# Kernel optimization log

Hardware: AMD Instinct MI355X
Metric: run time of the kernel (lower is better)

Reference implementation:

```python
import jax, jax.numpy as jnp
import numpy as np

B, T = 16, 512
S = T - 16  # sequence length after three 5x5 VALID convs and pool (H: T-4-4-4-5+1)
H = 64      # GRU hidden size


def setup_inputs() -> dict:
    key = jax.random.key(0)
    ks = jax.random.split(key, 20)
    def prm(k, shape, s=0.02):
        return jax.random.normal(k, shape, dtype=jnp.float32) * s
    return {
        "evaluation": jax.random.normal(ks[0], (B, 128, T), dtype=jnp.float32),
        "template":   jax.random.normal(ks[1], (B, 128, T), dtype=jnp.float32),
        "conv1_w": prm(ks[2], (16, 1, 5, 5), 0.05),  "conv1_b": prm(ks[3], (16,)),
        "conv2_w": prm(ks[4], (32, 16, 5, 5), 0.05), "conv2_b": prm(ks[5], (32,)),
        "conv3_w": prm(ks[6], (64, 32, 5, 5), 0.05), "conv3_b": prm(ks[7], (64,)),
        "lin1_w": prm(ks[8], (64, 3712)), "lin1_b": prm(ks[9], (64,)),
        "W_ih": prm(ks[10], (192, 64), 0.1), "W_hh": prm(ks[11], (192, 64), 0.1),
        "b_ih": prm(ks[12], (192,)),          "b_hh": prm(ks[13], (192,)),
        "att_w": prm(ks[14], (1, 64)),  "att_b": prm(ks[15], (1,)),
        "lin3_w": prm(ks[16], (128, 64)), "lin3_b": prm(ks[17], (128,)),
        "cls_w": prm(ks[18], (2, 128)),   "cls_b": prm(ks[19], (2,)),
    }


def _conv(x, w, b):
    # x: (N, C, H, W), w: (O, C, kh, kw), VALID, stride 1
    y = jax.lax.conv_general_dilated(x, w, (1, 1), 'VALID',
                                     dimension_numbers=('NCHW', 'OIHW', 'NCHW'))
    return y + b[None, :, None, None]


def _gru_seq(x, W_ih, W_hh, b_ih, b_hh):
    # x: (L, 64). One hidden state carried over the whole length (this mirrors
    # the torch module threading h0/h1 across samples in its Python loop).
    gi = x @ W_ih.T + b_ih  # (L, 192) input gates precomputed
    def step(h, gi_t):
        gh = W_hh @ h + b_hh
        r = jax.nn.sigmoid(gi_t[:H] + gh[:H])
        z = jax.nn.sigmoid(gi_t[H:2 * H] + gh[H:2 * H])
        n = jnp.tanh(gi_t[2 * H:] + r * gh[2 * H:])
        h_new = (1.0 - z) * n + z * h
        return h_new, h_new
    _, hs = jax.lax.scan(step, jnp.zeros((H,), x.dtype), gi)
    return hs  # (L, 64)


def reference(evaluation, template, conv1_w, conv1_b, conv2_w, conv2_b,
              conv3_w, conv3_b, lin1_w, lin1_b, W_ih, W_hh, b_ih, b_hh,
              att_w, att_b, lin3_w, lin3_b, cls_w, cls_b):
    # Shared conv trunk on stacked eval+template batch
    x = jnp.concatenate([evaluation, template], axis=0)      # (2B, 128, T)
    x = jnp.transpose(x, (0, 2, 1))[:, None]                 # (2B, 1, T, 128)
    x = _conv(x, conv1_w, conv1_b)                           # (2B, 16, T-4, 124)
    x = _conv(x, conv2_w, conv2_b)                           # (2B, 32, T-8, 120)
    x = _conv(x, conv3_w, conv3_b)                           # (2B, 64, T-12, 116)
    x = jax.lax.reduce_window(x, -jnp.inf, jax.lax.max,
                              (1, 1, 5, 2), (1, 1, 1, 2), 'VALID')  # (2B, 64, S, 58)
    # torch does a raw per-sample reshape (64, S, 58) -> (S, 3712)
    x = x.reshape(2 * B, S, 3712)
    x = x @ lin1_w.T + lin1_b                                # (2B, S, 64)
    # GRU: hidden carried across the batch -> one long scan per branch
    E = _gru_seq(x[:B].reshape(B * S, H), W_ih, W_hh, b_ih, b_hh).reshape(B, S, H)
    Tm = _gru_seq(x[B:].reshape(B * S, H), W_ih, W_hh, b_ih, b_hh).reshape(B, S, H)
    # alignment_weights[m, n] = <E[m], Tm[n]>, softmax over m (dim=0 per sample)
    A = jax.nn.softmax(jnp.einsum('bmd,bnd->bmn', E, Tm), axis=1)
    Tp = jnp.einsum('bmn,bnd->bmd', A, Tm)                   # template_prim
    dist = jnp.abs(Tp - E)                                    # (B, S, 64)
    att = jax.nn.softmax(jnp.einsum('bsd,d->bs', E, att_w[0]) + att_b[0], axis=1)
    rep = jnp.einsum('bs,bsd->bd', att, dist)                 # (B, 64)
    h = jax.nn.relu(rep)
    h = jax.nn.relu(h @ lin3_w.T + lin3_b)
    return h @ cls_w.T + cls_b                                # (B, 2)
```

## Files before the change

kernel.cpp:

```cpp
#include <hip/hip_runtime.h>
#include <hip/hip_bf16.h>
#include <math.h>


#define DEVI static __device__ __forceinline__
typedef __attribute__((ext_vector_type(8))) short short8;
typedef __attribute__((ext_vector_type(4))) float f32x4;
typedef __attribute__((ext_vector_type(8))) float f32x8;
typedef unsigned short ushort_t;

DEVI float fsig(float x)   { return 1.f / (1.f + __expf(-x)); }
DEVI float ftanh_(float x) { return 2.f / (1.f + __expf(-2.f * x)) - 1.f; }
DEVI float bf2f(ushort_t u) { union { unsigned int i; float f; } v; v.i = ((unsigned int)u) << 16; return v.f; }
DEVI ushort_t f2bf(float f) {
    union { float f; unsigned int i; } v; v.f = f;
    unsigned int r = v.i + 0x7FFF + ((v.i >> 16) & 1);
    return (ushort_t)(r >> 16);
}
DEVI f32x8 bf2f8(short8 s) {
    f32x8 r;
#pragma unroll
    for (int k = 0; k < 8; k++) r[k] = bf2f((ushort_t)s[k]);
    return r;
}
DEVI f32x8 max8(f32x8 a, f32x8 b) {
    f32x8 r;
#pragma unroll
    for (int k = 0; k < 8; k++) r[k] = fmaxf(a[k], b[k]);
    return r;
}

DEVI void glds16(const ushort_t* g, ushort_t* l)
{
    __builtin_amdgcn_global_load_lds(
        (const __attribute__((address_space(1))) void*)g,
        (__attribute__((address_space(3))) void*)l, 16, 0, 0);
}

__global__ void pack_w2(const float* __restrict__ w2, ushort_t* __restrict__ w2p)
{
    for (int idx = blockIdx.x * 256 + threadIdx.x; idx < 15360; idx += gridDim.x * 256) {
        int kh = idx / 3072, rem = idx % 3072;
        int kw = rem / 512;
        int co = (rem >> 4) & 31, ci = rem & 15;
        float v = (kw < 5) ? w2[((co * 16 + ci) * 5 + kh) * 5 + kw] : 0.f;
        w2p[idx] = f2bf(v);
    }
}
__global__ void pack_w3(const float* __restrict__ w3, ushort_t* __restrict__ w3p)
{
    for (int idx = blockIdx.x * 256 + threadIdx.x; idx < 51200; idx += gridDim.x * 256) {
        int kh = idx / 10240, rem = idx % 10240;
        int kw = rem / 2048;
        int co = (rem >> 5) & 63, ci = rem & 31;
        w3p[idx] = f2bf(w3[((co * 32 + ci) * 5 + kh) * 5 + kw]);
    }
}
__global__ void pack_l1w(const float* __restrict__ l1w, ushort_t* __restrict__ l1wp)
{
    for (int idx = blockIdx.x * 256 + threadIdx.x; idx < 262144; idx += gridDim.x * 256) {
        int n = idx >> 12, kp = idx & 4095;
        int r = kp >> 6, j = kp & 63;
        float v = (j < 58) ? l1w[n * 3712 + r * 58 + j] : 0.f;
        l1wp[idx] = f2bf(v);
    }
}

__global__ void conv1_kernel(const float* __restrict__ ev,
                             const float* __restrict__ tmpl,
                             const float* __restrict__ wgt,
                             const float* __restrict__ bias,
                             ushort_t* __restrict__ out, int n0)
{
    const int h0  = blockIdx.x * 4;
    const int w0  = blockIdx.y * 62;
    const int nl  = blockIdx.z;
    const int n   = n0 + nl;
    const int tid = threadIdx.x;
    const int wl  = tid & 63;
    const int cg  = tid >> 6;
    const float* src = (n < 16) ? (ev + (size_t)n * 65536)
                                : (tmpl + (size_t)(n - 16) * 65536);

    __shared__ float tin[8 * 68];
    __shared__ float tw[16 * 25];

    float acc[4][4];
#pragma unroll
    for (int j = 0; j < 4; j++)
#pragma unroll
        for (int hh = 0; hh < 4; hh++) acc[j][hh] = 0.f;

    for (int idx = tid; idx < 528; idx += 256) {
        int cc = idx >> 3, r = idx & 7;
        tin[r * 68 + cc] = src[(w0 + cc) * 512 + h0 + r];
    }
    for (int idx = tid; idx < 400; idx += 256) tw[idx] = wgt[idx];
    __syncthreads();
#pragma unroll
    for (int kh = 0; kh < 5; kh++) {
#pragma unroll
        for (int kw = 0; kw < 5; kw++) {
            float iv[4];
#pragma unroll
            for (int hh = 0; hh < 4; hh++)
                iv[hh] = tin[(hh + kh) * 68 + wl + kw];
#pragma unroll
            for (int j = 0; j < 4; j++) {
                float wv = tw[(cg * 4 + j) * 25 + kh * 5 + kw];
#pragma unroll
                for (int hh = 0; hh < 4; hh++)
                    acc[j][hh] = fmaf(wv, iv[hh], acc[j][hh]);
            }
        }
    }
    if (wl < 62) {
#pragma unroll
        for (int hh = 0; hh < 4; hh++) {
            ushort_t pk[4];
#pragma unroll
            for (int j = 0; j < 4; j++)
                pk[j] = f2bf(acc[j][hh] + bias[cg * 4 + j]);
            ushort_t* dst = out + ((size_t)(nl * 508 + h0 + hh) * 124 + w0 + wl) * 16 + cg * 4;
            *(uint2*)dst = *(uint2*)pk;
        }
    }
}

template<int CI, int CO, int NF, int MF, int NHI, int W_T, int KSTEPS,
         int KW_TOT, int H_IN, int W_IN, bool PAD2, bool HPOOL, int MAXB>
__global__ __launch_bounds__(256, MAXB) void conv_mfma(
    const ushort_t* __restrict__ in, const ushort_t* __restrict__ wpk,
    const float* __restrict__ bias, ushort_t* __restrict__ out)
{
    constexpr int H_OUT = H_IN - 4;
    constexpr int W_OUT = W_IN - 4;
    constexpr int HALO  = W_T + 6;
    constexpr int OCT   = CI / 8;
    constexpr int AROWS = 4 * NHI + 4;
    constexpr int APL   = AROWS * HALO;
    constexpr int BPL   = KW_TOT * CO;

    const int h0 = blockIdx.x * (4 * NHI);
    const int w0 = blockIdx.y * W_T;
    const int nl = blockIdx.z;
    const int tid  = threadIdx.x;
    const int wv   = tid >> 6;
    const int lane = tid & 63;
    const int l16  = lane & 15;
    const int kq   = lane >> 4;

    __shared__ __align__(16) ushort_t As[OCT * APL * 8];
    __shared__ __align__(16) ushort_t Bs[OCT * BPL * 8];

    f32x4 acc[NHI][MF][NF];
#pragma unroll
    for (int hi = 0; hi < NHI; hi++)
#pragma unroll
        for (int mi = 0; mi < MF; mi++)
#pragma unroll
            for (int ni = 0; ni < NF; ni++)
                acc[hi][mi][ni] = f32x4{0.f, 0.f, 0.f, 0.f};

    for (int idx = tid; idx < OCT * APL; idx += 256) {
        int oct = idx / APL, e = idx - oct * APL;
        int r = e / HALO, c = e - r * HALO;
        glds16(in + ((size_t)((nl * H_IN + h0 + r) * W_IN + w0 + c)) * CI + oct * 8,
               &As[idx * 8]);
    }

    const int aoct = PAD2 ? (kq & 1) : kq;
    const int kwq  = PAD2 ? (kq >> 1) : 0;

#pragma unroll
    for (int kh = 0; kh < 5; kh++) {
        __syncthreads();
        for (int idx = tid; idx < OCT * BPL; idx += 256) {
            int oct = idx / BPL, e = idx - oct * BPL;
            int kw = e / CO, co = e - kw * CO;
            glds16(wpk + ((size_t)((kh * KW_TOT + kw) * CO + co)) * CI + oct * 8,
                   &Bs[idx * 8]);
        }
        __syncthreads();
#pragma unroll
        for (int st = 0; st < KSTEPS; st++) {
            const int colq = (PAD2 ? st * 2 : st) + kwq;
            short8 bfv[NF];
#pragma unroll
            for (int ni = 0; ni < NF; ni++)
                bfv[ni] = *(const short8*)&Bs[(aoct * BPL + colq * CO + ni * 16 + l16) * 8];
#pragma unroll
            for (int hi = 0; hi < NHI; hi++) {
                short8 af[MF];
#pragma unroll
                for (int mi = 0; mi < MF; mi++)
                    af[mi] = *(const short8*)&As[(aoct * APL + (hi * 4 + wv + kh) * HALO + mi * 16 + l16 + colq) * 8];
#pragma unroll
                for (int mi = 0; mi < MF; mi++)
#pragma unroll
                    for (int ni = 0; ni < NF; ni++)
                        acc[hi][mi][ni] = __builtin_amdgcn_mfma_f32_16x16x32_bf16(
                            af[mi], bfv[ni], acc[hi][mi][ni], 0, 0, 0);
            }
        }
    }

#pragma unroll
    for (int hi = 0; hi < NHI; hi++) {
        const int h = h0 + hi * 4 + wv;
        if (h < H_OUT) {
#pragma unroll
            for (int mi = 0; mi < MF; mi++) {
#pragma unroll
                for (int ni = 0; ni < NF; ni++) {
                    int co = ni * 16 + l16;
                    float bv = bias[co];
                    if constexpr (HPOOL) {
                        const int jw = (w0 + mi * 16 + kq * 4) >> 1;
                        if (jw < 58)
                            out[((size_t)(nl * H_OUT + h) * 58 + jw) * CO + co] =
                                f2bf(fmaxf(acc[hi][mi][ni][0], acc[hi][mi][ni][1]) + bv);
                        if (jw + 1 < 58)
                            out[((size_t)(nl * H_OUT + h) * 58 + jw + 1) * CO + co] =
                                f2bf(fmaxf(acc[hi][mi][ni][2], acc[hi][mi][ni][3]) + bv);
                    } else {
#pragma unroll
                        for (int reg = 0; reg < 4; reg++) {
                            int w = w0 + mi * 16 + kq * 4 + reg;
                            if (w < W_OUT)
                                out[((size_t)(nl * H_OUT + h) * W_OUT + w) * CO + co] =
                                    f2bf(acc[hi][mi][ni][reg] + bv);
                        }
                    }
                }
            }
        }
    }
}

__global__ __launch_bounds__(512) void pool_fused(const ushort_t* __restrict__ a3h,
                                                  ushort_t* __restrict__ pooled)
{
    const int nl = blockIdx.y;
    const int s0 = blockIdx.x * 16;
    const int t  = threadIdx.x;
    __shared__ ushort_t L[4 * 3712];

    const int j = t >> 3, oct = t & 7;
    const ushort_t* base = a3h + (size_t)nl * 1856000 + (size_t)j * 64 + oct * 8;
    ushort_t* dst = pooled + (size_t)nl * 1841152;

#define LOADROW(rr) bf2f8(*(const short8*)(base + (size_t)(rr) * 3712))
    f32x8 w0, w1, w2v, w3v;
    if (t < 464) {
        w0  = LOADROW(s0);
        w1  = LOADROW(s0 + 1);
        w2v = LOADROW(s0 + 2);
        w3v = LOADROW(s0 + 3);
    }
    for (int g = 0; g < 4; g++) {
        if (t < 464) {
#pragma unroll
            for (int k = 0; k < 4; k++) {
                int s = s0 + g * 4 + k;
                f32x8 w4 = LOADROW(s + 4);
                f32x8 mx = max8(max8(max8(w0, w1), max8(w2v, w3v)), w4);
#pragma unroll
                for (int u = 0; u < 8; u++)
                    L[k * 3712 + (oct * 8 + u) * 58 + j] = f2bf(mx[u]);
                w0 = w1; w1 = w2v; w2v = w3v; w3v = w4;
            }
        }
        __syncthreads();
        const int sg = s0 + g * 4;
        for (int e = t; e < 14848; e += 512) {
            int k = e / 3712, r = e - k * 3712;
            int c = r / 58, jj = r - c * 58;
            dst[(size_t)c * 28768 + (sg + k) * 58 + jj] = L[e];
        }
        __syncthreads();
    }
#undef LOADROW
}

__global__ __launch_bounds__(256) void lin1_mfma(
    const ushort_t* __restrict__ pooled, const ushort_t* __restrict__ l1wp,
    float* __restrict__ xb, int n0, int RT)
{
    const int mt  = blockIdx.x;
    const int kqb = blockIdx.y;
    const int r0  = mt * 64;
    const int t   = threadIdx.x;
    const int wv  = t >> 6, lane = t & 63, l16 = lane & 15, kq = lane >> 4;

    __shared__ __align__(16) ushort_t As[8 * 64 * 8];
    __shared__ __align__(16) ushort_t Bs[8 * 64 * 8];

    f32x4 acc[4];
#pragma unroll
    for (int ni = 0; ni < 4; ni++) acc[ni] = f32x4{0.f, 0.f, 0.f, 0.f};

    for (int kb = 0; kb < 16; kb++) {
        const int k0 = kqb * 1024 + kb * 64;
        const int r  = k0 >> 6;
        __syncthreads();
        for (int idx = t; idx < 512; idx += 256) {
            int oct = idx >> 6, row = idx & 63;
            int rr = r0 + row;
            short8 v = short8{0, 0, 0, 0, 0, 0, 0, 0};
            if (rr < RT)
                v = *(const short8*)(pooled + (size_t)rr * 3712 + r * 58 + oct * 8);
            *(short8*)&As[idx * 8] = v;
        }
        for (int idx = t; idx < 512; idx += 256) {
            int oct = idx >> 6, co = idx & 63;
            *(short8*)&Bs[idx * 8] =
                *(const short8*)(l1wp + (size_t)co * 4096 + k0 + oct * 8);
        }
        __syncthreads();
#pragma unroll
        for (int st = 0; st < 2; st++) {
            short8 af = *(const short8*)&As[((st * 4 + kq) * 64 + wv * 16 + l16) * 8];
#pragma unroll
            for (int ni = 0; ni < 4; ni++) {
                short8 bfv = *(const short8*)&Bs[((st * 4 + kq) * 64 + ni * 16 + l16) * 8];
                acc[ni] = __builtin_amdgcn_mfma_f32_16x16x32_bf16(af, bfv, acc[ni], 0, 0, 0);
            }
        }
    }
#pragma unroll
    for (int ni = 0; ni < 4; ni++) {
        int co = ni * 16 + l16;
#pragma unroll
        for (int reg = 0; reg < 4; reg++) {
            int rr = r0 + wv * 16 + kq * 4 + reg;
            if (rr < RT)
                atomicAdd(&xb[((size_t)n0 * 496 + rr) * 64 + co], acc[ni][reg]);
        }
    }
}

__global__ __launch_bounds__(192) void gi_kernel(
    const float* __restrict__ x, const float* __restrict__ Wih,
    const float* __restrict__ bih, const float* __restrict__ l1b,
    float* __restrict__ gi)
{
    const int r0 = blockIdx.x * 64;
    const int j  = threadIdx.x;
    __shared__ float wls[192 * 65];
    __shared__ float xl[64 * 64];

    for (int idx = j; idx < 12288; idx += 192)
        wls[(idx >> 6) * 65 + (idx & 63)] = Wih[idx];
    for (int idx = j; idx < 4096; idx += 192)
        xl[idx] = x[(size_t)r0 * 64 + idx] + l1b[idx & 63];
    __syncthreads();

    float w[64];
#pragma unroll
    for (int d = 0; d < 64; d++) w[d] = wls[j * 65 + d];
    const float bj = bih[j];

    for (int s = 0; s < 64; s++) {
        float a = bj;
#pragma unroll
        for (int d = 0; d < 64; d++) a = fmaf(w[d], xl[s * 64 + d], a);
        gi[(size_t)(r0 + s) * 192 + j] = a;
    }
}

__global__ __launch_bounds__(192, 3) void gru_kernel(
    const float* __restrict__ gi, const float* __restrict__ Whh,
    const float* __restrict__ bhh, float* __restrict__ Eo,
    float* __restrict__ To)
{
    const int c  = blockIdx.x;
    const int br = (c >= 496) ? 1 : 0;
    const int q  = c - br * 496;
    const int j  = threadIdx.x;
    const float* gb = gi + (size_t)br * 7936 * 192;
    float* out = br ? To : Eo;

    float w[64];
#pragma unroll
    for (int k = 0; k < 64; k++) w[k] = Whh[j * 64 + k];
    const float bh = bhh[j];

    __shared__ __align__(16) float hs[64];
    __shared__ float gs[192];
    __shared__ float gnl[64];

    float h[64];
#pragma unroll
    for (int k = 0; k < 64; k++) h[k] = 0.f;
    float hown = 0.f;

    const int cs  = q * 16;
    int start = cs - 96;
    if (start < 0) start = 0;
    const int end = cs + 16;

    const bool isN  = (j >= 128);
    const bool isW0 = (j < 64);

    float pg[4];
#pragma unroll
    for (int u = 0; u < 4; u++) {
        int s = start + u;
        pg[u] = (s < end) ? gb[(size_t)s * 192 + j] : 0.f;
    }

    int s = start;
    while (s < end) {
#pragma unroll
        for (int u = 0; u < 4; u++) {
            if (s < end) {
                float g = pg[u];
                int sp = s + 4;
                if (sp < end) pg[u] = gb[(size_t)sp * 192 + j];
                float a0 = bh, a1 = 0.f;
#pragma unroll
                for (int k = 0; k < 64; k += 2) {
                    a0 = fmaf(w[k],     h[k],     a0);
                    a1 = fmaf(w[k + 1], h[k + 1], a1);
                }
                float gh = a0 + a1;
                gs[j] = isN ? gh : (gh + g);
                if (isN) gnl[j - 128] = g;
                __syncthreads();
                float hn = 0.f;
                if (isW0) {
                    float r  = fsig(gs[j]);
                    float z  = fsig(gs[64 + j]);
                    float nv = ftanh_(gnl[j] + r * gs[128 + j]);
                    hn = (1.f - z) * nv + z * hown;
                    hown = hn;
                    hs[j] = hn;
                }
                __syncthreads();
#pragma unroll
                for (int k = 0; k < 16; k++) {
                    float4 v = ((const float4*)hs)[k];
                    h[4 * k + 0] = v.x; h[4 * k + 1] = v.y;
                    h[4 * k + 2] = v.z; h[4 * k + 3] = v.w;
                }
                if (isW0 && s >= cs) out[(size_t)s * 64 + j] = hn;
                s++;
            }
        }
    }
}

__global__ void scores_kernel(const float* __restrict__ E,
                              const float* __restrict__ Tm,
                              float* __restrict__ S)
{
    const int b  = blockIdx.z;
    const int m0 = blockIdx.y * 32;
    const int n0 = blockIdx.x * 64;
    const int t  = threadIdx.x;
    const int nl = t & 63, mg = t >> 6;
    __shared__ float El[32 * 64];
    __shared__ float Tms[64 * 65];

    for (int idx = t; idx < 2048; idx += 256) {
        int r = idx >> 6, d = idx & 63;
        int m = m0 + r;
        El[idx] = (m < 496) ? E[((size_t)b * 496 + m) * 64 + d] : 0.f;
    }
    for (int idx = t; idx < 4096; idx += 256) {
        int r = idx >> 6, d = idx & 63;
        int n = n0 + r;
        Tms[d * 65 + r] = (n < 496) ? Tm[((size_t)b * 496 + n) * 64 + d] : 0.f;
    }
    __syncthreads();

    float acc[8];
#pragma unroll
    for (int j = 0; j < 8; j++) acc[j] = 0.f;
#pragma unroll 4
    for (int d = 0; d < 64; d++) {
        float tv = Tms[d * 65 + nl];
#pragma unroll
        for (int j = 0; j < 8; j++)
            acc[j] = fmaf(El[(mg * 8 + j) * 64 + d], tv, acc[j]);
    }
    int n = n0 + nl;
    if (n < 496) {
#pragma unroll
        for (int j = 0; j < 8; j++) {
            int m = m0 + mg * 8 + j;
            if (m < 496) S[((size_t)b * 496 + m) * 496 + n] = acc[j];
        }
    }
}

__global__ void colsum_kernel(const float* __restrict__ S,
                              float* __restrict__ invZ)
{
    const int b  = blockIdx.y;
    const int n0 = blockIdx.x * 32;
    const int t  = threadIdx.x;
    const int c  = t & 31, rg = t >> 5;
    const int n  = n0 + c;
    float sum = 0.f;
    if (n < 496) {
        const float* base = S + (size_t)b * 246016 + n;
        for (int mm = rg * 62; mm < rg * 62 + 62; mm++)
            sum += __expf(base[(size_t)mm * 496]);
    }
    __shared__ float red[256];
    red[t] = sum;
    __syncthreads();
    if (t < 32) {
        float s = 0.f;
#pragma unroll
        for (int g = 0; g < 8; g++) s += red[g * 32 + t];
        if (n0 + t < 496) invZ[b * 496 + n0 + t] = 1.f / s;
    }
}

__global__ void tp_kernel(const float* __restrict__ S,
                          const float* __restrict__ Tm,
                          const float* __restrict__ invZ,
                          float* __restrict__ Tp)
{
    const int b  = blockIdx.y;
    const int m0 = blockIdx.x * 32;
    const int t  = threadIdx.x;
    const int d  = t & 63, mg = t >> 6;
    __shared__ float As2[32 * 128];
    __shared__ float Ts[128 * 64];
    float acc[8];
#pragma unroll
    for (int j = 0; j < 8; j++) acc[j] = 0.f;

    for (int nc = 0; nc < 512; nc += 128) {
        __syncthreads();
        for (int idx = t; idx < 4096; idx += 256) {
            int r = idx >> 7, cc = idx & 127;
            int m = m0 + r, n = nc + cc;
            As2[idx] = (m < 496 && n < 496)
                          ? __expf(S[((size_t)b * 496 + m) * 496 + n]) : 0.f;
        }
        for (int idx = t; idx < 8192; idx += 256) {
            int r = idx >> 6, dd = idx & 63;
            int n = nc + r;
            Ts[idx] = (n < 496)
                          ? Tm[((size_t)b * 496 + n) * 64 + dd] * invZ[b * 496 + n]
                          : 0.f;
        }
        __syncthreads();
#pragma unroll 4
        for (int nn = 0; nn < 128; nn++) {
            float tv = Ts[nn * 64 + d];
#pragma unroll
            for (int j = 0; j < 8; j++)
                acc[j] = fmaf(As2[(mg * 8 + j) * 128 + nn], tv, acc[j]);
        }
    }
#pragma unroll
    for (int j = 0; j < 8; j++) {
        int m = m0 + mg * 8 + j;
        if (m < 496) Tp[((size_t)b * 496 + m) * 64 + d] = acc[j];
    }
}

__global__ void attrep_kernel(const float* __restrict__ E,
                              const float* __restrict__ Tp,
                              const float* __restrict__ attw,
                              const float* __restrict__ attb,
                              float* __restrict__ rep)
{
    const int b = blockIdx.x;
    const int t = threadIdx.x;
    __shared__ float aw[64];
    __shared__ float lg[496];
    __shared__ float att[496];
    __shared__ float redm[4], reds[4];
    __shared__ float part[256];

    if (t < 64) aw[t] = attw[t];
    __syncthreads();
    for (int s = t; s < 496; s += 256) {
        const float* Er = E + ((size_t)b * 496 + s) * 64;
        float a = 0.f;
#pragma unroll
        for (int dd = 0; dd < 64; dd++) a = fmaf(Er[dd], aw[dd], a);
        lg[s] = a + attb[0];
    }
    __syncthreads();
    float m = -1e30f;
    for (int s = t; s < 496; s += 256) m = fmaxf(m, lg[s]);
    for (int off = 32; off > 0; off >>= 1)
        m = fmaxf(m, __shfl_xor(m, off, 64));
    if ((t & 63) == 0) redm[t >> 6] = m;
    __syncthreads();
    m = fmaxf(fmaxf(redm[0], redm[1]), fmaxf(redm[2], redm[3]));
    float sum = 0.f;
    for (int s = t; s < 496; s += 256) {
        float e = __expf(lg[s] - m);
        att[s] = e;
        sum += e;
    }
    for (int off = 32; off > 0; off >>= 1) sum += __shfl_xor(sum, off, 64);
    if ((t & 63) == 0) reds[t >> 6] = sum;
    __syncthreads();
    float inv = 1.f / (reds[0] + reds[1] + reds[2] + reds[3]);

    const int d = t & 63, sg = t >> 6;
    float p = 0.f;
    for (int k = 0; k < 124; k++) {
        int s = sg + 4 * k;
        size_t o = ((size_t)b * 496 + s) * 64 + d;
        p = fmaf(att[s] * inv, fabsf(Tp[o] - E[o]), p);
    }
    part[t] = p;
    __syncthreads();
    if (t < 64)
        rep[b * 64 + t] = part[t] + part[64 + t] + part[128 + t] + part[192 + t];
}

__global__ void mlp_kernel(const float* __restrict__ rep,
                           const float* __restrict__ W3,
                           const float* __restrict__ b3,
                           const float* __restrict__ Wc,
                           const float* __restrict__ bc,
                           float* __restrict__ out)
{
    const int b = blockIdx.x;
    const int t = threadIdx.x;
    __shared__ float hr[64];
    __shared__ float h2[128];
    if (t < 64) hr[t] = fmaxf(rep[b * 64 + t], 0.f);
    __syncthreads();
    float a = b3[t];
#pragma unroll
    for (int d = 0; d < 64; d++) a = fmaf(W3[t * 64 + d], hr[d], a);
    h2[t] = fmaxf(a, 0.f);
    __syncthreads();
    if (t < 2) {
        float o = bc[t];
        for (int k = 0; k < 128; k++) o = fmaf(Wc[t * 128 + k], h2[k], o);
        out[b * 2 + t] = o;
    }
}

extern "C" void kernel_launch(void* const* d_in, const int* in_sizes, int n_in,
                              void* d_out, int out_size, void* d_ws,
                              size_t ws_size, hipStream_t stream)
{
    const float* ev   = (const float*)d_in[0];
    const float* tmpl = (const float*)d_in[1];
    const float* w1   = (const float*)d_in[2];
    const float* b1   = (const float*)d_in[3];
    const float* w2   = (const float*)d_in[4];
    const float* b2   = (const float*)d_in[5];
    const float* w3   = (const float*)d_in[6];
    const float* b3   = (const float*)d_in[7];
    const float* l1w  = (const float*)d_in[8];
    const float* l1b  = (const float*)d_in[9];
    const float* wih  = (const float*)d_in[10];
    const float* whh  = (const float*)d_in[11];
    const float* bih  = (const float*)d_in[12];
    const float* bhh  = (const float*)d_in[13];
    const float* attw = (const float*)d_in[14];
    const float* attb = (const float*)d_in[15];
    const float* l3w  = (const float*)d_in[16];
    const float* l3b  = (const float*)d_in[17];
    const float* clw  = (const float*)d_in[18];
    const float* clb  = (const float*)d_in[19];

    float* ws = (float*)d_ws;
    float* xb    = ws;
    float* Eb    = xb + 1015808ull;
    float* Tb    = Eb + 507904ull;
    float* Tpb   = Tb + 507904ull;
    float* repb  = Tpb + 507904ull;
    float* w2pf  = repb + 1024ull;
    float* w3pf  = w2pf + 7680ull;
    float* l1wpf = w3pf + 25600ull;
    float* invZb = l1wpf + 131072ull;
    float* arena = invZb + 8192ull;
    const size_t PERSIST = 2713088ull;

    ushort_t* w2p  = (ushort_t*)w2pf;
    ushort_t* w3p  = (ushort_t*)w3pf;
    ushort_t* l1wp = (ushort_t*)l1wpf;

    const int cand[6] = {32, 16, 8, 4, 2, 1};
    int C = 0;
    for (int ci = 0; ci < 6; ci++) {
        size_t a = (size_t)cand[ci] * 2823680ull + 16384ull;
        if (a < 3936256ull) a = 3936256ull;
        if ((PERSIST + a) * sizeof(float) <= ws_size) { C = cand[ci]; break; }
    }
    if (C == 0) return;

    float*    S1 = arena;
    float*    S2 = arena + (size_t)C * 967680ull + 8192ull;
    float*    gib = arena;
    float*    Sb  = arena;

    ushort_t* a2  = (ushort_t*)S1;
    ushort_t* pooled = (ushort_t*)S1;
    ushort_t* a1  = (ushort_t*)S2;
    ushort_t* a3h = (ushort_t*)S2;

    hipMemsetAsync(xb, 0, 1015808ull * sizeof(float), stream);
    pack_w2<<<15, 256, 0, stream>>>(w2, w2p);
    pack_w3<<<50, 256, 0, stream>>>(w3, w3p);
    pack_l1w<<<256, 256, 0, stream>>>(l1w, l1wp);

    const int RT = C * 496;
    const int mtiles = (RT + 63) / 64;

    for (int n0 = 0; n0 < 32; n0 += C) {
        conv1_kernel<<<dim3(127, 2, C), 256, 0, stream>>>(ev, tmpl, w1, b1, a1, n0);
        conv_mfma<16, 32, 2, 4, 2, 64, 3, 6, 508, 124, true, false, 4>
            <<<dim3(63, 2, C), 256, 0, stream>>>(a1, w2p, b2, a2);
        conv_mfma<32, 64, 4, 2, 2, 32, 5, 5, 504, 120, false, true, 3>
            <<<dim3(63, 4, C), 256, 0, stream>>>(a2, w3p, b3, a3h);
        pool_fused<<<dim3(31, C), 512, 0, stream>>>(a3h, pooled);
        lin1_mfma<<<dim3(mtiles, 4), 256, 0, stream>>>(pooled, l1wp, xb, n0, RT);
    }

    gi_kernel<<<248, 192, 0, stream>>>(xb, wih, bih, l1b, gib);
    gru_kernel<<<992, 192, 0, stream>>>(gib, whh, bhh, Eb, Tb);

    scores_kernel<<<dim3(8, 16, 16), 256, 0, stream>>>(Eb, Tb, Sb);
    colsum_kernel<<<dim3(16, 16), 256, 0, stream>>>(Sb, invZb);
    tp_kernel<<<dim3(16, 16), 256, 0, stream>>>(Sb, Tb, invZb, Tpb);

    attrep_kernel<<<16, 256, 0, stream>>>(Eb, Tpb, attw, attb, repb);
    mlp_kernel<<<16, 128, 0, stream>>>(repb, l3w, l3b, clw, clb,
                                       (float*)d_out);
}
```

Before: 773.0 us.

## Double-buffer conv weight tiles in LDS and split kernel-column stages

The weight slab for each conv kernel row is now loaded into one of two LDS buffers while the MFMA loop consumes the other. This removes one of the two barriers per stage. A new STPS parameter splits each kernel row into sub-stages so that conv3 can stage one kernel column at a time, which shrinks its per-buffer LDS footprint. The conv3 occupancy hint is raised from 3 to 4 blocks per CU, at the cost of more stages and barriers for conv3 and doubled B-buffer LDS for conv2.

Measured after the change: 784.9 us. Within noise of the previous version (+1.5%).

```diff
diff --git a/kernel.cpp b/kernel.cpp
--- a/kernel.cpp
+++ b/kernel.cpp
@@ -128,7 +128,7 @@
 }
 
 template<int CI, int CO, int NF, int MF, int NHI, int W_T, int KSTEPS,
-         int KW_TOT, int H_IN, int W_IN, bool PAD2, bool HPOOL, int MAXB>
+         int KW_TOT, int STPS, int H_IN, int W_IN, bool PAD2, bool HPOOL, int MAXB>
 __global__ __launch_bounds__(256, MAXB) void conv_mfma(
     const ushort_t* __restrict__ in, const ushort_t* __restrict__ wpk,
     const float* __restrict__ bias, ushort_t* __restrict__ out)
@@ -139,7 +139,9 @@
     constexpr int OCT   = CI / 8;
     constexpr int AROWS = 4 * NHI + 4;
     constexpr int APL   = AROWS * HALO;
-    constexpr int BPL   = KW_TOT * CO;
+    constexpr int BSTW  = KW_TOT / STPS;
+    constexpr int BPL   = BSTW * CO;
+    constexpr int NSG   = 5 * STPS;
 
     const int h0 = blockIdx.x * (4 * NHI);
     const int w0 = blockIdx.y * W_T;
@@ -151,7 +153,7 @@
     const int kq   = lane >> 4;
 
     __shared__ __align__(16) ushort_t As[OCT * APL * 8];
-    __shared__ __align__(16) ushort_t Bs[OCT * BPL * 8];
+    __shared__ __align__(16) ushort_t Bs[2][OCT * BPL * 8];
 
     f32x4 acc[NHI][MF][NF];
 #pragma unroll
@@ -168,33 +170,44 @@
         glds16(in + ((size_t)((nl * H_IN + h0 + r) * W_IN + w0 + c)) * CI + oct * 8,
                &As[idx * 8]);
     }
+    for (int idx = tid; idx < OCT * BPL; idx += 256) {
+        int oct = idx / BPL, e = idx - oct * BPL;
+        int kw = e / CO, co = e - kw * CO;
+        glds16(wpk + ((size_t)(kw * CO + co)) * CI + oct * 8, &Bs[0][idx * 8]);
+    }
+    __syncthreads();
 
     const int aoct = PAD2 ? (kq & 1) : kq;
     const int kwq  = PAD2 ? (kq >> 1) : 0;
 
 #pragma unroll
-    for (int kh = 0; kh < 5; kh++) {
-        __syncthreads();
-        for (int idx = tid; idx < OCT * BPL; idx += 256) {
-            int oct = idx / BPL, e = idx - oct * BPL;
-            int kw = e / CO, co = e - kw * CO;
-            glds16(wpk + ((size_t)((kh * KW_TOT + kw) * CO + co)) * CI + oct * 8,
-                   &Bs[idx * 8]);
-        }
-        __syncthreads();
-#pragma unroll
-        for (int st = 0; st < KSTEPS; st++) {
-            const int colq = (PAD2 ? st * 2 : st) + kwq;
+    for (int sg = 0; sg < NSG; ++sg) {
+        const int buf = sg & 1;
+        const int kh  = sg / STPS;
+        const int kw0 = (sg - kh * STPS) * BSTW;
+        if (sg + 1 < NSG) {
+            const int kh2  = (sg + 1) / STPS;
+            const int kw02 = ((sg + 1) - kh2 * STPS) * BSTW;
+            for (int idx = tid; idx < OCT * BPL; idx += 256) {
+                int oct = idx / BPL, e = idx - oct * BPL;
+                int kw = e / CO, co = e - kw * CO;
+                glds16(wpk + ((size_t)((kh2 * KW_TOT + kw02 + kw) * CO + co)) * CI + oct * 8,
+                       &Bs[buf ^ 1][idx * 8]);
+            }
+        }
+#pragma unroll
+        for (int st = 0; st < KSTEPS; ++st) {
+            const int wc = PAD2 ? (st * 2 + kwq) : st;
             short8 bfv[NF];
 #pragma unroll
             for (int ni = 0; ni < NF; ni++)
-                bfv[ni] = *(const short8*)&Bs[(aoct * BPL + colq * CO + ni * 16 + l16) * 8];
+                bfv[ni] = *(const short8*)&Bs[buf][(aoct * BPL + wc * CO + ni * 16 + l16) * 8];
 #pragma unroll
             for (int hi = 0; hi < NHI; hi++) {
                 short8 af[MF];
 #pragma unroll
                 for (int mi = 0; mi < MF; mi++)
-                    af[mi] = *(const short8*)&As[(aoct * APL + (hi * 4 + wv + kh) * HALO + mi * 16 + l16 + colq) * 8];
+                    af[mi] = *(const short8*)&As[(aoct * APL + (hi * 4 + wv + kh) * HALO + mi * 16 + l16 + kw0 + wc) * 8];
 #pragma unroll
                 for (int mi = 0; mi < MF; mi++)
 #pragma unroll
@@ -203,6 +216,7 @@
                             af[mi], bfv[ni], acc[hi][mi][ni], 0, 0, 0);
             }
         }
+        __syncthreads();
     }
 
 #pragma unroll
@@ -717,9 +731,9 @@
 
     for (int n0 = 0; n0 < 32; n0 += C) {
         conv1_kernel<<<dim3(127, 2, C), 256, 0, stream>>>(ev, tmpl, w1, b1, a1, n0);
-        conv_mfma<16, 32, 2, 4, 2, 64, 3, 6, 508, 124, true, false, 4>
+        conv_mfma<16, 32, 2, 4, 2, 64, 3, 6, 1, 508, 124, true, false, 4>
             <<<dim3(63, 2, C), 256, 0, stream>>>(a1, w2p, b2, a2);
-        conv_mfma<32, 64, 4, 2, 2, 32, 5, 5, 504, 120, false, true, 3>
+        conv_mfma<32, 64, 4, 2, 2, 32, 1, 5, 5, 504, 120, false, true, 4>
             <<<dim3(63, 4, C), 256, 0, stream>>>(a2, w3p, b3, a3h);
         pool_fused<<<dim3(31, C), 512, 0, stream>>>(a3h, pooled);
         lin1_mfma<<<dim3(mtiles, 4), 256, 0, stream>>>(pooled, l1wp, xb, n0, RT);
```
